# Kernel tuning notes

Hardware: AMD Instinct MI355X
Metric: run time of the kernel (lower is better)

## Reference

```python
import jax, jax.numpy as jnp
import numpy as np

PATCH_SIZE = 16
PATCH_STRIDE = 8
LEVEL = 3

# pywt db4 decomposition filters (dec_lo, dec_hi)
_DB4_DEC_LO = np.array([-0.010597401784997278, 0.032883011666982945,
                        0.030841381835986965, -0.18703481171888114,
                        -0.02798376941698385, 0.6308807679295904,
                        0.7148465705525415, 0.23037781330885523], dtype=np.float32)
_DB4_DEC_HI = np.array([-0.23037781330885523, 0.7148465705525415,
                        -0.6308807679295904, -0.02798376941698385,
                        0.18703481171888114, 0.030841381835986965,
                        -0.032883011666982945, -0.010597401784997278], dtype=np.float32)


def _swt(x, level):
    """Undecimated (a-trous) SWT with periodic boundary, ptwt convention.
    x: (BN, T) with T divisible by 2**level. Returns [cA_L, cD_L, ..., cD_1]."""
    # torch conv1d is cross-correlation -> use flipped filters (true convolution)
    filt = jnp.stack([jnp.asarray(_DB4_DEC_LO[::-1].copy()),
                      jnp.asarray(_DB4_DEC_HI[::-1].copy())], axis=0)[:, None, :]  # (2,1,8)
    filt = filt.astype(x.dtype)
    flen = filt.shape[-1]
    res_lo = x[:, None, :]  # (BN, 1, T)
    details = []
    for lvl in range(level):
        d = 2 ** lvl
        padl, padr = d * (flen // 2 - 1), d * (flen // 2)
        xp = jnp.concatenate([res_lo[..., -padl:], res_lo, res_lo[..., :padr]], axis=-1)
        res = jax.lax.conv_general_dilated(
            xp, filt, window_strides=(1,), padding='VALID',
            rhs_dilation=(d,), dimension_numbers=('NCH', 'OIH', 'NCH'))  # (BN,2,T)
        res_lo = res[:, :1, :]
        details.append(res[:, 1, :])
    return [res_lo[:, 0, :]] + details[::-1]


def setup_inputs() -> dict:
    key = jax.random.key(0)
    x = jax.random.normal(key, (64, 4096, 32), dtype=jnp.float32)
    return {"x": x}


def reference(x):
    B, T, N = x.shape
    xt = jnp.transpose(x, (0, 2, 1))  # (B, N, T)
    pow2 = 2 ** LEVEL
    pad_len = (-T) % pow2
    if pad_len:
        xt = jnp.pad(xt, ((0, 0), (0, 0), (0, pad_len)), mode='edge')  # replicate
    T_pad = T + pad_len
    coeffs = _swt(xt.reshape(B * N, T_pad), LEVEL)           # (level+1) x (BN, T_pad)
    cs = jnp.stack(coeffs, axis=1).reshape(B, N, LEVEL + 1, T_pad)
    if pad_len:
        cs = cs[..., :T]
    P = (T - PATCH_SIZE) // PATCH_STRIDE + 1
    idx = jnp.arange(P)[:, None] * PATCH_STRIDE + jnp.arange(PATCH_SIZE)[None, :]
    patches = cs[..., idx]                                   # (B, N, L+1, P, p)
    patches = jnp.transpose(patches, (0, 3, 1, 2, 4))        # (B, P, N, L+1, p)
    return patches.reshape(B * P, N * (LEVEL + 1), PATCH_SIZE)
```

## Files before the change

kernel.cpp:

```cpp
#include <hip/hip_runtime.h>


#define NTHREADS 256
#define T_MASK   4095

#define S_ST 76
#define ST_C 2436
#define LDS_FLOATS (4 * ST_C)

__device__ __constant__ float c_lo[8] = {
    -0.010597401784997278f, 0.032883011666982945f, 0.030841381835986965f,
    -0.18703481171888114f, -0.02798376941698385f, 0.6308807679295904f,
    0.7148465705525415f,   0.23037781330885523f};
__device__ __constant__ float c_hi[8] = {
    -0.23037781330885523f, 0.7148465705525415f, -0.6308807679295904f,
    -0.02798376941698385f, 0.18703481171888114f, 0.030841381835986965f,
    -0.032883011666982945f, -0.010597401784997278f};

__global__ __launch_bounds__(NTHREADS, 2) void swt_patch(const float* __restrict__ x,
                                                         float* __restrict__ out) {
    __shared__ float lds[LDS_FLOATS];

    const int blk = blockIdx.x;
    const int b   = blk >> 6;
    const int cid = blk & 63;
    const int T0  = cid << 6;
    const int p0  = cid << 3;
    const int tid = threadIdx.x;
    const int n   = tid & 31;
    const int s   = tid >> 5;
    const int t0  = 9 * s;

    const float* xb = x + (size_t)b * (4096 * 32) + n;

    float xw[58];
    if (cid != 0 && cid != 63) {
        const float* xp = xb + (size_t)(T0 + t0 - 21) * 32;
#pragma unroll
        for (int i = 0; i < 58; ++i) xw[i] = xp[(size_t)i * 32];
    } else {
#pragma unroll
        for (int i = 0; i < 58; ++i) {
            const int t = (T0 + t0 - 21 + i) & T_MASK;
            xw[i] = xb[(size_t)t * 32];
        }
    }

    {
        float d1[9];
#pragma unroll
        for (int m = 0; m < 9; ++m) {
            float sd = 0.f;
#pragma unroll
            for (int j = 0; j < 8; ++j) sd = fmaf(c_hi[j], xw[m + 25 - j], sd);
            d1[m] = sd;
        }
#pragma unroll
        for (int m = 0; m < 9; ++m) lds[3 * ST_C + n * S_ST + t0 + m] = d1[m];
    }

    float a1[51];
#pragma unroll
    for (int k = 0; k < 51; ++k) {
        float sa = 0.f;
#pragma unroll
        for (int j = 0; j < 8; ++j) sa = fmaf(c_lo[j], xw[k + 7 - j], sa);
        a1[k] = sa;
    }

    {
        float d2[9];
#pragma unroll
        for (int m = 0; m < 9; ++m) {
            float sd = 0.f;
#pragma unroll
            for (int j = 0; j < 8; ++j) sd = fmaf(c_hi[j], a1[m + 26 - 2 * j], sd);
            d2[m] = sd;
        }
#pragma unroll
        for (int m = 0; m < 9; ++m) lds[2 * ST_C + n * S_ST + t0 + m] = d2[m];
    }

    float a2[37];
#pragma unroll
    for (int m2 = 0; m2 < 37; ++m2) {
        float sa = 0.f;
#pragma unroll
        for (int j = 0; j < 8; ++j) sa = fmaf(c_lo[j], a1[m2 + 14 - 2 * j], sa);
        a2[m2] = sa;
    }

#pragma unroll
    for (int m = 0; m < 9; ++m) {
        float sa = 0.f, sd = 0.f;
#pragma unroll
        for (int j = 0; j < 8; ++j) {
            const float v = a2[m + 28 - 4 * j];
            sa = fmaf(c_lo[j], v, sa);
            sd = fmaf(c_hi[j], v, sd);
        }
        lds[0 * ST_C + n * S_ST + t0 + m] = sa;
        lds[1 * ST_C + n * S_ST + t0 + m] = sd;
    }
    __syncthreads();

    float4* out4 = (float4*)(out + ((size_t)b * 511 + p0) * 2048);
#pragma unroll
    for (int it = 0; it < 16; ++it) {
        const int e4 = tid + it * NTHREADS;
        const int p_local = e4 >> 9;
        if (p0 + p_local < 511) {
            const int nn = (e4 >> 4) & 31;
            const int c  = (e4 >> 2) & 3;
            const int trel = 8 * p_local + 4 * (e4 & 3);
            out4[e4] = *(const float4*)&lds[c * ST_C + nn * S_ST + trel];
        }
    }
}

extern "C" void kernel_launch(void* const* d_in, const int* in_sizes, int n_in,
                              void* d_out, int out_size, void* d_ws, size_t ws_size,
                              hipStream_t stream) {
    const float* x = (const float*)d_in[0];
    float* out = (float*)d_out;
    hipLaunchKernelGGL(swt_patch, dim3(64 * 64), dim3(NTHREADS), 0, stream, x, out);
}
```

Before: 289.0 us.

## Make blocks persistent over eight chunks with double-buffered LDS staging

Each block now handles eight consecutive time chunks of a batch in a loop instead of one, and the grid shrinks from 4096 to 512 blocks. It alternates between two LDS staging buffers, so with one barrier per iteration the next chunk's compute can overlap the previous chunk's output stores. This doubles LDS use per block to about 78 KB, which may reduce how many blocks fit per CU. With 512 blocks on a GPU of roughly 256 CUs, the kernel risks underfilling the device and losing latency hiding.

```diff
diff --git a/kernel.cpp b/kernel.cpp
--- a/kernel.cpp
+++ b/kernel.cpp
@@ -6,7 +6,8 @@
 
 #define S_ST 76
 #define ST_C 2436
-#define LDS_FLOATS (4 * ST_C)
+#define BUF_FLOATS (4 * ST_C)
+#define LDS_FLOATS (2 * BUF_FLOATS)
 
 __device__ __constant__ float c_lo[8] = {
     -0.010597401784997278f, 0.032883011666982945f, 0.030841381835986965f,
@@ -21,99 +22,105 @@
                                                          float* __restrict__ out) {
     __shared__ float lds[LDS_FLOATS];
 
-    const int blk = blockIdx.x;
-    const int b   = blk >> 6;
-    const int cid = blk & 63;
-    const int T0  = cid << 6;
-    const int p0  = cid << 3;
-    const int tid = threadIdx.x;
-    const int n   = tid & 31;
-    const int s   = tid >> 5;
-    const int t0  = 9 * s;
+    const int g    = blockIdx.x;
+    const int b    = g >> 3;
+    const int cid0 = (g & 7) << 3;
+    const int tid  = threadIdx.x;
+    const int n    = tid & 31;
+    const int s    = tid >> 5;
+    const int t0   = 9 * s;
 
     const float* xb = x + (size_t)b * (4096 * 32) + n;
+    float4* outb = (float4*)out + (size_t)b * 511 * 512;
 
-    float xw[58];
-    if (cid != 0 && cid != 63) {
-        const float* xp = xb + (size_t)(T0 + t0 - 21) * 32;
+    for (int k = 0; k < 8; ++k) {
+        const int cid = cid0 + k;
+        const int T0  = cid << 6;
+        float* stg = lds + (k & 1) * BUF_FLOATS;
+
+        float xw[58];
+        if (cid != 0 && cid != 63) {
+            const float* xp = xb + (size_t)(T0 + t0 - 21) * 32;
 #pragma unroll
-        for (int i = 0; i < 58; ++i) xw[i] = xp[(size_t)i * 32];
-    } else {
+            for (int i = 0; i < 58; ++i) xw[i] = xp[(size_t)i * 32];
+        } else {
 #pragma unroll
-        for (int i = 0; i < 58; ++i) {
-            const int t = (T0 + t0 - 21 + i) & T_MASK;
-            xw[i] = xb[(size_t)t * 32];
+            for (int i = 0; i < 58; ++i) {
+                const int t = (T0 + t0 - 21 + i) & T_MASK;
+                xw[i] = xb[(size_t)t * 32];
+            }
         }
-    }
 
-    {
-        float d1[9];
+        {
+            float d1[9];
+#pragma unroll
+            for (int m = 0; m < 9; ++m) {
+                float sd = 0.f;
+#pragma unroll
+                for (int j = 0; j < 8; ++j) sd = fmaf(c_hi[j], xw[m + 25 - j], sd);
+                d1[m] = sd;
+            }
+#pragma unroll
+            for (int m = 0; m < 9; ++m) stg[3 * ST_C + n * S_ST + t0 + m] = d1[m];
+        }
+
+        float a1[51];
+#pragma unroll
+        for (int k1 = 0; k1 < 51; ++k1) {
+            float sa = 0.f;
+#pragma unroll
+            for (int j = 0; j < 8; ++j) sa = fmaf(c_lo[j], xw[k1 + 7 - j], sa);
+            a1[k1] = sa;
+        }
+
+        {
+            float d2[9];
+#pragma unroll
+            for (int m = 0; m < 9; ++m) {
+                float sd = 0.f;
+#pragma unroll
+                for (int j = 0; j < 8; ++j) sd = fmaf(c_hi[j], a1[m + 26 - 2 * j], sd);
+                d2[m] = sd;
+            }
+#pragma unroll
+            for (int m = 0; m < 9; ++m) stg[2 * ST_C + n * S_ST + t0 + m] = d2[m];
+        }
+
+        float a2[37];
+#pragma unroll
+        for (int m2 = 0; m2 < 37; ++m2) {
+            float sa = 0.f;
+#pragma unroll
+            for (int j = 0; j < 8; ++j) sa = fmaf(c_lo[j], a1[m2 + 14 - 2 * j], sa);
+            a2[m2] = sa;
+        }
+
 #pragma unroll
         for (int m = 0; m < 9; ++m) {
-            float sd = 0.f;
+            float sa = 0.f, sd = 0.f;
 #pragma unroll
-            for (int j = 0; j < 8; ++j) sd = fmaf(c_hi[j], xw[m + 25 - j], sd);
-            d1[m] = sd;
+            for (int j = 0; j < 8; ++j) {
+                const float v = a2[m + 28 - 4 * j];
+                sa = fmaf(c_lo[j], v, sa);
+                sd = fmaf(c_hi[j], v, sd);
+            }
+            stg[0 * ST_C + n * S_ST + t0 + m] = sa;
+            stg[1 * ST_C + n * S_ST + t0 + m] = sd;
         }
+        __syncthreads();
+
+        const int p0 = cid << 3;
+        float4* out4 = outb + (size_t)p0 * 512;
 #pragma unroll
-        for (int m = 0; m < 9; ++m) lds[3 * ST_C + n * S_ST + t0 + m] = d1[m];
-    }
-
-    float a1[51];
-#pragma unroll
-    for (int k = 0; k < 51; ++k) {
-        float sa = 0.f;
-#pragma unroll
-        for (int j = 0; j < 8; ++j) sa = fmaf(c_lo[j], xw[k + 7 - j], sa);
-        a1[k] = sa;
-    }
-
-    {
-        float d2[9];
-#pragma unroll
-        for (int m = 0; m < 9; ++m) {
-            float sd = 0.f;
-#pragma unroll
-            for (int j = 0; j < 8; ++j) sd = fmaf(c_hi[j], a1[m + 26 - 2 * j], sd);
-            d2[m] = sd;
-        }
-#pragma unroll
-        for (int m = 0; m < 9; ++m) lds[2 * ST_C + n * S_ST + t0 + m] = d2[m];
-    }
-
-    float a2[37];
-#pragma unroll
-    for (int m2 = 0; m2 < 37; ++m2) {
-        float sa = 0.f;
-#pragma unroll
-        for (int j = 0; j < 8; ++j) sa = fmaf(c_lo[j], a1[m2 + 14 - 2 * j], sa);
-        a2[m2] = sa;
-    }
-
-#pragma unroll
-    for (int m = 0; m < 9; ++m) {
-        float sa = 0.f, sd = 0.f;
-#pragma unroll
-        for (int j = 0; j < 8; ++j) {
-            const float v = a2[m + 28 - 4 * j];
-            sa = fmaf(c_lo[j], v, sa);
-            sd = fmaf(c_hi[j], v, sd);
-        }
-        lds[0 * ST_C + n * S_ST + t0 + m] = sa;
-        lds[1 * ST_C + n * S_ST + t0 + m] = sd;
-    }
-    __syncthreads();
-
-    float4* out4 = (float4*)(out + ((size_t)b * 511 + p0) * 2048);
-#pragma unroll
-    for (int it = 0; it < 16; ++it) {
-        const int e4 = tid + it * NTHREADS;
-        const int p_local = e4 >> 9;
-        if (p0 + p_local < 511) {
-            const int nn = (e4 >> 4) & 31;
-            const int c  = (e4 >> 2) & 3;
-            const int trel = 8 * p_local + 4 * (e4 & 3);
-            out4[e4] = *(const float4*)&lds[c * ST_C + nn * S_ST + trel];
+        for (int it = 0; it < 16; ++it) {
+            const int e4 = tid + it * NTHREADS;
+            const int p_local = e4 >> 9;
+            if (p0 + p_local < 511) {
+                const int nn = (e4 >> 4) & 31;
+                const int c  = (e4 >> 2) & 3;
+                const int trel = 8 * p_local + 4 * (e4 & 3);
+                out4[e4] = *(const float4*)&stg[c * ST_C + nn * S_ST + trel];
+            }
         }
     }
 }
@@ -123,5 +130,5 @@
                               hipStream_t stream) {
     const float* x = (const float*)d_in[0];
     float* out = (float*)d_out;
-    hipLaunchKernelGGL(swt_patch, dim3(64 * 64), dim3(NTHREADS), 0, stream, x, out);
+    hipLaunchKernelGGL(swt_patch, dim3(512), dim3(NTHREADS), 0, stream, x, out);
 }
```

Result: slower. 300.3 us (+3.9%).
